# Optimization experiments

Hardware: AMD Instinct MI355X
Metric: run time of the kernel (lower is better)

The kernel has to match this reference:

```python
import jax, jax.numpy as jnp
import numpy as np

N_NODES = 50000
N_EDGES = 1600000
HIDDEN = 128
IN_DIM = 3  # x (1) + relative pos (2)


def setup_inputs() -> dict:
    key = jax.random.key(0)
    ks = jax.random.split(key, 5)
    x = jax.random.normal(ks[0], (N_NODES, 1), dtype=jnp.float32)
    pos = jax.random.normal(ks[1], (N_NODES, 2), dtype=jnp.float32)
    # MLP params (Linear(3,128) -> ReLU -> Linear(128,128)), fan-in scaled
    W1 = jax.random.normal(ks[2], (IN_DIM, HIDDEN), dtype=jnp.float32) / np.sqrt(IN_DIM)
    b1 = jnp.zeros((HIDDEN,), dtype=jnp.float32)
    W2 = jax.random.normal(ks[3], (HIDDEN, HIDDEN), dtype=jnp.float32) / np.sqrt(HIDDEN)
    b2 = jnp.zeros((HIDDEN,), dtype=jnp.float32)
    edge_index = jax.random.randint(ks[4], (2, N_EDGES), 0, N_NODES, dtype=jnp.int64)
    return {"x": x, "pos": pos, "W1": W1, "b1": b1, "W2": W2, "b2": b2,
            "edge_index": edge_index}


def reference(x, pos, W1, b1, W2, b2, edge_index):
    # PTConv with aggr='add': per-edge message = nn(cat([x_j, pos_j - pos_i]))
    # then scatter-add into destination node i.
    src = edge_index[0]  # j (neighbor / source)
    dst = edge_index[1]  # i (center / destination)
    msg_in = jnp.concatenate([x[src], pos[src] - pos[dst]], axis=-1)  # [E, 3]
    h = jax.nn.relu(msg_in @ W1 + b1) @ W2 + b2                        # [E, 128]
    out = jax.ops.segment_sum(h, dst, num_segments=x.shape[0])        # [N, 128]
    return out
```

## Files before the change

kernel.cpp:

```cpp
#include <hip/hip_runtime.h>


#define HIDDEN 128
#define BNODES 16
#define BSH 4
#define SUPSH 10
#define CAPA 36864
#define CAPF 768
#define EPBA 2048
#define SThrA 512
#define KSUB 16
#define SThrB 512
#define W2LD 136

typedef float v2f __attribute__((ext_vector_type(2)));
typedef short bf16x8 __attribute__((ext_vector_type(8)));
typedef float f32x4 __attribute__((ext_vector_type(4)));

__device__ __forceinline__ unsigned cvt_pk_bf16(float lo, float hi) {
    unsigned r;
    asm("v_cvt_pk_bf16_f32 %0, %1, %2" : "=v"(r) : "v"(lo), "v"(hi));
    return r;
}

__device__ __forceinline__ unsigned short f2bf(float f) {
    unsigned int u = __float_as_uint(f);
    u += 0x7fffu + ((u >> 16) & 1u);
    return (unsigned short)(u >> 16);
}

__global__ __launch_bounds__(SThrA) void k_scatA(const int* __restrict__ src,
                                                 const int* __restrict__ dst,
                                                 int* __restrict__ bcurA,
                                                 unsigned int* __restrict__ pairsA,
                                                 int E, int NSUP) {
    __shared__ int h[64];
    __shared__ int hb[64];
    int tid = threadIdx.x;
    if (tid < 64) h[tid] = 0;
    __syncthreads();
    int base = blockIdx.x * EPBA;
    int lim = base + EPBA; if (lim > E) lim = E;
    int n = lim - base;
    int n4 = ((E & 3) == 0) ? (n >> 2) : 0;
    const int4* d4 = (const int4*)(dst + base);
    const int4* s4 = (const int4*)(src + base);
    for (int i = tid; i < n4; i += SThrA) {
        int4 d = d4[i];
        atomicAdd(&h[d.x >> SUPSH], 1);
        atomicAdd(&h[d.y >> SUPSH], 1);
        atomicAdd(&h[d.z >> SUPSH], 1);
        atomicAdd(&h[d.w >> SUPSH], 1);
    }
    for (int i = base + (n4 << 2) + tid; i < lim; i += SThrA)
        atomicAdd(&h[dst[i] >> SUPSH], 1);
    __syncthreads();
    if (tid < 64) {
        int c = h[tid];
        hb[tid] = (c && tid < NSUP) ? atomicAdd(&bcurA[tid], c) : 0;
        h[tid] = 0;
    }
    __syncthreads();
#define PUTA(dd, ss) { int sb = (dd) >> SUPSH; int loc = hb[sb] + atomicAdd(&h[sb], 1); \
        if (loc < CAPA) pairsA[sb * CAPA + loc] = ((unsigned)(ss) << SUPSH) | (unsigned)((dd) & 1023); }
    for (int i = tid; i < n4; i += SThrA) {
        int4 d = d4[i];
        int4 s = s4[i];
        PUTA(d.x, s.x) PUTA(d.y, s.y) PUTA(d.z, s.z) PUTA(d.w, s.w)
    }
    for (int i = base + (n4 << 2) + tid; i < lim; i += SThrA) {
        int dd = dst[i], ss = src[i];
        PUTA(dd, ss)
    }
#undef PUTA
}

__global__ __launch_bounds__(SThrB) void k_scatB(const int* __restrict__ bcurA,
                                                 const unsigned int* __restrict__ pairsA,
                                                 int* __restrict__ bcurF,
                                                 unsigned int* __restrict__ pairsF,
                                                 int NB) {
    __shared__ int h[64];
    __shared__ int hb[64];
    int tid = threadIdx.x;
    int s = blockIdx.x / KSUB;
    int k = blockIdx.x % KSUB;
    int base0 = s * CAPA;
    int ec = bcurA[s]; if (ec > CAPA) ec = CAPA;
    int slice = (((ec + KSUB - 1) / KSUB) + 3) & ~3;
    int lo = base0 + k * slice;
    int e1 = base0 + ec;
    int hi = lo + slice; if (hi > e1) hi = e1;
    int n = hi - lo; if (n < 0) n = 0;
    int n4 = n >> 2;
    const uint4* p4 = (const uint4*)(pairsA + lo);
    if (tid < 64) h[tid] = 0;
    __syncthreads();
    for (int i = tid; i < n4; i += SThrB) {
        uint4 e = p4[i];
        atomicAdd(&h[(e.x >> BSH) & 63u], 1);
        atomicAdd(&h[(e.y >> BSH) & 63u], 1);
        atomicAdd(&h[(e.z >> BSH) & 63u], 1);
        atomicAdd(&h[(e.w >> BSH) & 63u], 1);
    }
    for (int i = lo + (n4 << 2) + tid; i < hi; i += SThrB)
        atomicAdd(&h[(pairsA[i] >> BSH) & 63u], 1);
    __syncthreads();
    if (tid < 64) {
        int c = h[tid];
        int fb = s * 64 + tid;
        hb[tid] = (c && fb < NB) ? atomicAdd(&bcurF[fb], c) : 0;
        h[tid] = 0;
    }
    __syncthreads();
#define PUTB(ee) { int fbl = (int)(((ee) >> BSH) & 63u); int fb = s * 64 + fbl; \
        int loc = hb[fbl] + atomicAdd(&h[fbl], 1); \
        if (fb < NB && loc < CAPF) pairsF[(size_t)fb * CAPF + loc] = (((ee) >> SUPSH) << BSH) | ((ee) & 15u); }
    for (int i = tid; i < n4; i += SThrB) {
        uint4 e = p4[i];
        PUTB(e.x) PUTB(e.y) PUTB(e.z) PUTB(e.w)
    }
    for (int i = lo + (n4 << 2) + tid; i < hi; i += SThrB) {
        unsigned int e = pairsA[i];
        PUTB(e)
    }
#undef PUTB
}

__global__ __launch_bounds__(256) void k_main(const float* __restrict__ x,
                                              const float* __restrict__ pos,
                                              const float* __restrict__ W1,
                                              const float* __restrict__ b1,
                                              const int* __restrict__ bcurF,
                                              const unsigned int* __restrict__ pairs,
                                              float* __restrict__ agg,
                                              int* __restrict__ deg, int N) {
    __shared__ uint2 f_s[CAPF];
    __shared__ int cnt[BNODES];
    __shared__ int offn[BNODES + 1];
    __shared__ int cur[BNODES];

    int tid = threadIdx.x, lane = tid & 63, w = tid >> 6;
    int b = blockIdx.x;
    int n0 = b * BNODES;
    int e0 = b * CAPF;
    int ec = bcurF[b]; if (ec > CAPF) ec = CAPF;

    int c0 = 2 * lane;
    v2f w10 = { W1[c0],              W1[c0 + 1] };
    v2f w11 = { W1[HIDDEN + c0],     W1[HIDDEN + c0 + 1] };
    v2f w12 = { W1[2 * HIDDEN + c0], W1[2 * HIDDEN + c0 + 1] };
    v2f b1v = { b1[c0], b1[c0 + 1] };
    const v2f zero = { 0.f, 0.f };
    const float2* pos2 = (const float2*)pos;

    if (tid < BNODES) cnt[tid] = 0;
    __syncthreads();
    unsigned int rr0 = 0, rr1 = 0, rr2 = 0;
    if (tid + 0 * 256 < ec) rr0 = pairs[e0 + tid + 0 * 256];
    if (tid + 1 * 256 < ec) rr1 = pairs[e0 + tid + 1 * 256];
    if (tid + 2 * 256 < ec) rr2 = pairs[e0 + tid + 2 * 256];
    if (tid + 0 * 256 < ec) atomicAdd(&cnt[rr0 & 15u], 1);
    if (tid + 1 * 256 < ec) atomicAdd(&cnt[rr1 & 15u], 1);
    if (tid + 2 * 256 < ec) atomicAdd(&cnt[rr2 & 15u], 1);
    __syncthreads();
    if (tid < BNODES) {
        int v = cnt[tid];
        int sc = v;
        #pragma unroll
        for (int d = 1; d < BNODES; d <<= 1) {
            int u = __shfl_up(sc, d);
            if (lane >= d) sc += u;
        }
        offn[tid + 1] = sc;
        if (tid == 0) offn[0] = 0;
        cur[tid] = sc - v;
    }
    __syncthreads();
    #pragma unroll
    for (int q = 0; q < 3; ++q) {
        unsigned int r = q == 0 ? rr0 : q == 1 ? rr1 : rr2;
        if (tid + q * 256 < ec) {
            int j = (int)(r >> BSH);
            int local = (int)(r & 15u);
            float a = x[j];
            float2 pj = pos2[j];
            float2 pi = pos2[n0 + local];
            unsigned pk = cvt_pk_bf16(pj.x - pi.x, pj.y - pi.y);
            int p = atomicAdd(&cur[local], 1);
            f_s[p] = make_uint2(pk, __float_as_uint(a));
        }
    }
    __syncthreads();
    v2f acc[4];
    int dga[4];
    #pragma unroll
    for (int s = 0; s < 4; ++s) {
        int l = w * 4 + s;
        int sb = offn[l], se = offn[l + 1];
        dga[s] = se - sb;
        v2f A = zero;
        #pragma unroll 4
        for (int t = sb; t < se; ++t) {
            uint2 r = f_s[t];
            float rx = __uint_as_float(r.x << 16);
            float ry = __uint_as_float(r.x & 0xffff0000u);
            float a  = __uint_as_float(r.y);
            v2f h = a * w10 + b1v;
            h = rx * w11 + h;
            h = ry * w12 + h;
            h = __builtin_elementwise_max(h, zero);
            A += h;
        }
        acc[s] = A;
    }

    #pragma unroll
    for (int s = 0; s < 4; ++s) {
        int l = w * 4 + s;
        int node = n0 + l;
        if (node < N) {
            ((v2f*)&agg[(size_t)node * HIDDEN])[lane] = acc[s];
            if (lane == 0) deg[node] = dga[s];
        }
    }
}

__global__ __launch_bounds__(256) void k_w2(float* __restrict__ agg,
                                            const float* __restrict__ W2,
                                            const float* __restrict__ b2,
                                            const int* __restrict__ deg, int N) {
    __shared__ unsigned short w2t[HIDDEN * W2LD];
    int tid = threadIdx.x;
    for (int idx = tid; idx < HIDDEN * HIDDEN; idx += 256) {
        int k = idx >> 7, c = idx & 127;
        w2t[c * W2LD + k] = f2bf(W2[idx]);
    }
    __syncthreads();

    int lane = tid & 63, w = tid >> 6;
    int row0 = blockIdx.x * 64 + w * 16;
    if (row0 >= N) return;

    int rA = row0 + (lane & 15);
    int koff = (lane >> 4) * 8;
    bool okA = rA < N;

    bf16x8 a[4];
    #pragma unroll
    for (int k0 = 0; k0 < 4; ++k0) {
        float4 fa = {0.f,0.f,0.f,0.f}, fb = {0.f,0.f,0.f,0.f};
        if (okA) {
            const float4* p = (const float4*)&agg[(size_t)rA * HIDDEN + k0 * 32 + koff];
            fa = p[0]; fb = p[1];
        }
        union { uint4 u; bf16x8 v; } cv;
        cv.u.x = cvt_pk_bf16(fa.x, fa.y);
        cv.u.y = cvt_pk_bf16(fa.z, fa.w);
        cv.u.z = cvt_pk_bf16(fb.x, fb.y);
        cv.u.w = cvt_pk_bf16(fb.z, fb.w);
        a[k0] = cv.v;
    }

    f32x4 acc[8];
    #pragma unroll
    for (int ct = 0; ct < 8; ++ct) acc[ct] = (f32x4){0.f,0.f,0.f,0.f};

    #pragma unroll
    for (int ct = 0; ct < 8; ++ct) {
        int col = ct * 16 + (lane & 15);
        #pragma unroll
        for (int k0 = 0; k0 < 4; ++k0) {
            bf16x8 bfrag = *(const bf16x8*)&w2t[col * W2LD + k0 * 32 + koff];
            acc[ct] = __builtin_amdgcn_mfma_f32_16x16x32_bf16(a[k0], bfrag, acc[ct], 0, 0, 0);
        }
    }

    int mbase = row0 + (lane >> 4) * 4;
    float dg[4];
    #pragma unroll
    for (int i = 0; i < 4; ++i) dg[i] = (mbase + i < N) ? (float)deg[mbase + i] : 0.f;

    #pragma unroll
    for (int ct = 0; ct < 8; ++ct) {
        int col = ct * 16 + (lane & 15);
        float b2c = b2[col];
        #pragma unroll
        for (int i = 0; i < 4; ++i) {
            int r = mbase + i;
            if (r < N) agg[(size_t)r * HIDDEN + col] = acc[ct][i] + dg[i] * b2c;
        }
    }
}

extern "C" void kernel_launch(void* const* d_in, const int* in_sizes, int n_in,
                              void* d_out, int out_size, void* d_ws, size_t ws_size,
                              hipStream_t stream) {
    const float* x   = (const float*)d_in[0];
    const float* pos = (const float*)d_in[1];
    const float* W1  = (const float*)d_in[2];
    const float* b1  = (const float*)d_in[3];
    const float* W2  = (const float*)d_in[4];
    const float* b2  = (const float*)d_in[5];
    const int*   ei  = (const int*)d_in[6];

    int N = in_sizes[0];
    int E = in_sizes[6] / 2;
    const int* src = ei;
    const int* dst = ei + E;
    float* out = (float*)d_out;

    int NB   = (N + BNODES - 1) / BNODES;
    int NSUP = (N + 1023) >> SUPSH;

    int* bcurA = (int*)d_ws;
    int* bcurF = bcurA + 64;
    int* deg   = bcurF + NB;
    unsigned int* pairsA = (unsigned int*)(deg + N);
    unsigned int* pairsF = pairsA + (size_t)NSUP * CAPA;

    int gribsA = (E + EPBA - 1) / EPBA;

    hipMemsetAsync(bcurA, 0, (64 + (size_t)NB) * sizeof(int), stream);
    k_scatA<<<gribsA, SThrA, 0, stream>>>(src, dst, bcurA, pairsA, E, NSUP);
    k_scatB<<<NSUP * KSUB, SThrB, 0, stream>>>(bcurA, pairsA, bcurF, pairsF, NB);
    k_main<<<NB, 256, 0, stream>>>(x, pos, W1, b1, bcurF, pairsF, out, deg, N);
    k_w2<<<(N + 63) / 64, 256, 0, stream>>>(out, W2, b2, deg, N);
}
```

Measured before the change: 99.71 us.

## Split bucket scatter into histogram/scan/place and pack node features as float4

Replaces the single atomic-reservation scatter kernel with a histogram pass, a one-block prefix scan, and a placement pass that writes to deterministic offsets. The histogram pass also packs x and pos into a float4 array so the main kernel gathers each source node with one load. The destination position term is folded into a per-node bias outside the edge loop. This adds two kernel launches and a second read of dst, and it rounds absolute rather than relative positions to bf16, which may reduce accuracy.

Measured after the change: 138.7 us. 1.39x slower.

```diff
diff --git a/kernel.cpp b/kernel.cpp
--- a/kernel.cpp
+++ b/kernel.cpp
@@ -8,7 +8,6 @@
 #define CAPA 36864
 #define CAPF 768
 #define EPBA 2048
-#define SThrA 512
 #define KSUB 16
 #define SThrB 512
 #define W2LD 136
@@ -29,15 +28,70 @@
     return (unsigned short)(u >> 16);
 }
 
-__global__ __launch_bounds__(SThrA) void k_scatA(const int* __restrict__ src,
-                                                 const int* __restrict__ dst,
-                                                 int* __restrict__ bcurA,
-                                                 unsigned int* __restrict__ pairsA,
-                                                 int E, int NSUP) {
+__global__ __launch_bounds__(256) void k_histA(const int* __restrict__ dst,
+                                               const float* __restrict__ x,
+                                               const float* __restrict__ pos,
+                                               int* __restrict__ histA,
+                                               float4* __restrict__ xpos,
+                                               int E, int N) {
+    __shared__ int h[64];
+    int tid = threadIdx.x;
+    if (tid < 64) h[tid] = 0;
+    int nb = blockIdx.x * 64 + tid;
+    if (tid < 64 && nb < N) {
+        float2 p = ((const float2*)pos)[nb];
+        xpos[nb] = make_float4(x[nb], p.x, p.y, 0.f);
+    }
+    __syncthreads();
+    int base = blockIdx.x * EPBA;
+    int lim = base + EPBA; if (lim > E) lim = E;
+    int n = lim - base;
+    int n4 = ((E & 3) == 0) ? (n >> 2) : 0;
+    const int4* d4 = (const int4*)(dst + base);
+    for (int i = tid; i < n4; i += 256) {
+        int4 d = d4[i];
+        atomicAdd(&h[d.x >> SUPSH], 1);
+        atomicAdd(&h[d.y >> SUPSH], 1);
+        atomicAdd(&h[d.z >> SUPSH], 1);
+        atomicAdd(&h[d.w >> SUPSH], 1);
+    }
+    for (int i = base + (n4 << 2) + tid; i < lim; i += 256)
+        atomicAdd(&h[dst[i] >> SUPSH], 1);
+    __syncthreads();
+    if (tid < 64) histA[blockIdx.x * 64 + tid] = h[tid];
+}
+
+__global__ __launch_bounds__(256) void k_scanA(int* __restrict__ histA,
+                                               int* __restrict__ bcurA, int NBLK) {
+    __shared__ int csum[4][64];
+    int tid = threadIdx.x;
+    int s = tid & 63, c = tid >> 6;
+    int chk = (NBLK + 3) >> 2;
+    int b0 = c * chk, b1 = b0 + chk; if (b1 > NBLK) b1 = NBLK;
+    int sum = 0;
+    for (int b = b0; b < b1; ++b) sum += histA[b * 64 + s];
+    csum[c][s] = sum;
+    __syncthreads();
+    if (tid < 64) {
+        int run = tid * CAPA;
+        #pragma unroll
+        for (int c2 = 0; c2 < 4; ++c2) { int t = csum[c2][tid]; csum[c2][tid] = run; run += t; }
+        bcurA[tid] = run - tid * CAPA;
+    }
+    __syncthreads();
+    int run = csum[c][s];
+    for (int b = b0; b < b1; ++b) { int t = histA[b * 64 + s]; histA[b * 64 + s] = run; run += t; }
+}
+
+__global__ __launch_bounds__(256) void k_placeA(const int* __restrict__ src,
+                                                const int* __restrict__ dst,
+                                                const int* __restrict__ histA,
+                                                unsigned int* __restrict__ pairsA,
+                                                int E) {
     __shared__ int h[64];
     __shared__ int hb[64];
     int tid = threadIdx.x;
-    if (tid < 64) h[tid] = 0;
+    if (tid < 64) { hb[tid] = histA[blockIdx.x * 64 + tid]; h[tid] = 0; }
     __syncthreads();
     int base = blockIdx.x * EPBA;
     int lim = base + EPBA; if (lim > E) lim = E;
@@ -45,30 +99,14 @@
     int n4 = ((E & 3) == 0) ? (n >> 2) : 0;
     const int4* d4 = (const int4*)(dst + base);
     const int4* s4 = (const int4*)(src + base);
-    for (int i = tid; i < n4; i += SThrA) {
-        int4 d = d4[i];
-        atomicAdd(&h[d.x >> SUPSH], 1);
-        atomicAdd(&h[d.y >> SUPSH], 1);
-        atomicAdd(&h[d.z >> SUPSH], 1);
-        atomicAdd(&h[d.w >> SUPSH], 1);
-    }
-    for (int i = base + (n4 << 2) + tid; i < lim; i += SThrA)
-        atomicAdd(&h[dst[i] >> SUPSH], 1);
-    __syncthreads();
-    if (tid < 64) {
-        int c = h[tid];
-        hb[tid] = (c && tid < NSUP) ? atomicAdd(&bcurA[tid], c) : 0;
-        h[tid] = 0;
-    }
-    __syncthreads();
-#define PUTA(dd, ss) { int sb = (dd) >> SUPSH; int loc = hb[sb] + atomicAdd(&h[sb], 1); \
-        if (loc < CAPA) pairsA[sb * CAPA + loc] = ((unsigned)(ss) << SUPSH) | (unsigned)((dd) & 1023); }
-    for (int i = tid; i < n4; i += SThrA) {
+#define PUTA(dd, ss) { int sb = (dd) >> SUPSH; int slot = hb[sb] + atomicAdd(&h[sb], 1); \
+        if (slot < (sb + 1) * CAPA) pairsA[slot] = ((unsigned)(ss) << SUPSH) | (unsigned)((dd) & 1023); }
+    for (int i = tid; i < n4; i += 256) {
         int4 d = d4[i];
         int4 s = s4[i];
         PUTA(d.x, s.x) PUTA(d.y, s.y) PUTA(d.z, s.z) PUTA(d.w, s.w)
     }
-    for (int i = base + (n4 << 2) + tid; i < lim; i += SThrA) {
+    for (int i = base + (n4 << 2) + tid; i < lim; i += 256) {
         int dd = dst[i], ss = src[i];
         PUTA(dd, ss)
     }
@@ -127,8 +165,7 @@
 #undef PUTB
 }
 
-__global__ __launch_bounds__(256) void k_main(const float* __restrict__ x,
-                                              const float* __restrict__ pos,
+__global__ __launch_bounds__(256) void k_main(const float4* __restrict__ xpos,
                                               const float* __restrict__ W1,
                                               const float* __restrict__ b1,
                                               const int* __restrict__ bcurF,
@@ -152,7 +189,6 @@
     v2f w12 = { W1[2 * HIDDEN + c0], W1[2 * HIDDEN + c0 + 1] };
     v2f b1v = { b1[c0], b1[c0 + 1] };
     const v2f zero = { 0.f, 0.f };
-    const float2* pos2 = (const float2*)pos;
 
     if (tid < BNODES) cnt[tid] = 0;
     __syncthreads();
@@ -183,12 +219,10 @@
         if (tid + q * 256 < ec) {
             int j = (int)(r >> BSH);
             int local = (int)(r & 15u);
-            float a = x[j];
-            float2 pj = pos2[j];
-            float2 pi = pos2[n0 + local];
-            unsigned pk = cvt_pk_bf16(pj.x - pi.x, pj.y - pi.y);
+            float4 f = xpos[j];
+            unsigned pk = cvt_pk_bf16(f.y, f.z);
             int p = atomicAdd(&cur[local], 1);
-            f_s[p] = make_uint2(pk, __float_as_uint(a));
+            f_s[p] = make_uint2(pk, __float_as_uint(f.x));
         }
     }
     __syncthreads();
@@ -197,18 +231,23 @@
     #pragma unroll
     for (int s = 0; s < 4; ++s) {
         int l = w * 4 + s;
+        int node = n0 + l;
         int sb = offn[l], se = offn[l + 1];
         dga[s] = se - sb;
+        float4 pi = (node < N) ? xpos[node] : make_float4(0.f, 0.f, 0.f, 0.f);
+        v2f t = pi.z * w12;
+        t = pi.y * w11 + t;
+        v2f bb = b1v - t;
         v2f A = zero;
         #pragma unroll 4
-        for (int t = sb; t < se; ++t) {
-            uint2 r = f_s[t];
-            float rx = __uint_as_float(r.x << 16);
-            float ry = __uint_as_float(r.x & 0xffff0000u);
+        for (int tt = sb; tt < se; ++tt) {
+            uint2 r = f_s[tt];
+            float px = __uint_as_float(r.x << 16);
+            float py = __uint_as_float(r.x & 0xffff0000u);
             float a  = __uint_as_float(r.y);
-            v2f h = a * w10 + b1v;
-            h = rx * w11 + h;
-            h = ry * w12 + h;
+            v2f h = a * w10 + bb;
+            h = px * w11 + h;
+            h = py * w12 + h;
             h = __builtin_elementwise_max(h, zero);
             A += h;
         }
@@ -312,18 +351,24 @@
 
     int NB   = (N + BNODES - 1) / BNODES;
     int NSUP = (N + 1023) >> SUPSH;
+    int NBLK = (E + EPBA - 1) / EPBA;
 
     int* bcurA = (int*)d_ws;
     int* bcurF = bcurA + 64;
     int* deg   = bcurF + NB;
-    unsigned int* pairsA = (unsigned int*)(deg + N);
+    int* histA = deg + N;
+    float4* xpos = (float4*)(histA + (size_t)NBLK * 64);
+    unsigned int* pairsA = (unsigned int*)(xpos + ((N + 63) & ~63));
     unsigned int* pairsF = pairsA + (size_t)NSUP * CAPA;
 
-    int gribsA = (E + EPBA - 1) / EPBA;
-
-    hipMemsetAsync(bcurA, 0, (64 + (size_t)NB) * sizeof(int), stream);
-    k_scatA<<<gribsA, SThrA, 0, stream>>>(src, dst, bcurA, pairsA, E, NSUP);
+    int nblk_nodes = (N + 63) / 64;
+    int gribsA = NBLK > nblk_nodes ? NBLK : nblk_nodes;
+
+    hipMemsetAsync(bcurF, 0, (size_t)NB * sizeof(int), stream);
+    k_histA<<<gribsA, 256, 0, stream>>>(dst, x, pos, histA, xpos, E, N);
+    k_scanA<<<1, 256, 0, stream>>>(histA, bcurA, NBLK);
+    k_placeA<<<NBLK, 256, 0, stream>>>(src, dst, histA, pairsA, E);
     k_scatB<<<NSUP * KSUB, SThrB, 0, stream>>>(bcurA, pairsA, bcurF, pairsF, NB);
-    k_main<<<NB, 256, 0, stream>>>(x, pos, W1, b1, bcurF, pairsF, out, deg, N);
+    k_main<<<NB, 256, 0, stream>>>(xpos, W1, b1, bcurF, pairsF, out, deg, N);
     k_w2<<<(N + 63) / 64, 256, 0, stream>>>(out, W2, b2, deg, N);
 }
```
